# Performance work log

Hardware: AMD Instinct MI355X
Metric: run time of the kernel (lower is better)

The kernel has to match this reference:

```python
import jax, jax.numpy as jnp
import numpy as np

B, S, E = 2, 2048, 4096
H = 16
D = E // H  # 256
MP = 4
ROTARY_DIM = 64
N_POS = 2048


def create_sinusoidal_positions(num_pos, dim):
    inv_freq = 1.0 / (10000.0 ** (jnp.arange(0, dim, 2, dtype=jnp.float32) / dim))
    sinusoid = jnp.einsum('i,j->ij', jnp.arange(num_pos, dtype=jnp.float32), inv_freq)
    return jnp.concatenate([jnp.sin(sinusoid), jnp.cos(sinusoid)], axis=1)  # [num_pos, dim]


def rotate_every_two(x):
    x1 = x[..., ::2]
    x2 = x[..., 1::2]
    return jnp.stack((-x2, x1), axis=-1).reshape(x.shape)


def apply_rotary_pos_emb(t, sin, cos):
    # sin, cos: [B, S, rot/2] -> [B, S, 1, rot] via repeat_interleave(2)
    sin = jnp.repeat(sin[:, :, None, :], 2, axis=-1)
    cos = jnp.repeat(cos[:, :, None, :], 2, axis=-1)
    return t * cos + rotate_every_two(t) * sin


def setup_inputs() -> dict:
    key = jax.random.key(0)
    k1, k2, k3 = jax.random.split(key, 3)
    hidden_states = jax.random.normal(k1, (B, S, E), dtype=jnp.float32) * 0.02
    w_qkv = jax.random.normal(k2, (E, 3 * E), dtype=jnp.float32) * 0.02
    w_out = jax.random.normal(k3, (E, E), dtype=jnp.float32) * 0.02
    position_ids = jnp.tile(jnp.arange(S, dtype=jnp.int32)[None, :], (B, 1))
    return {"hidden_states": hidden_states, "w_qkv": w_qkv, "w_out": w_out,
            "position_ids": position_ids}


def reference(hidden_states, w_qkv, w_out, position_ids):
    qkv = jnp.einsum('bse,ef->bsf', hidden_states, w_qkv)  # [B,S,3E]
    # Moss layout: reshape to mp_num chunks, split order is (query, value, key)
    qkv_split = qkv.reshape(B, S, MP, 3 * E // MP)
    local = D * H // MP
    query = qkv_split[..., :local]
    value = qkv_split[..., local:2 * local]
    key = qkv_split[..., 2 * local:]

    def split_heads(x):  # [B,S,MP,local] -> [B,S,H,D]
        return x.reshape(B, S, MP, H // MP, D).reshape(B, S, H, D)

    query, key, value = split_heads(query), split_heads(key), split_heads(value)

    embed_positions = create_sinusoidal_positions(N_POS, ROTARY_DIM)
    sincos = embed_positions[position_ids]  # [B,S,ROTARY_DIM]
    sin, cos = jnp.split(sincos, 2, axis=-1)

    q_rot = apply_rotary_pos_emb(query[..., :ROTARY_DIM], sin, cos)
    k_rot = apply_rotary_pos_emb(key[..., :ROTARY_DIM], sin, cos)
    query = jnp.concatenate([q_rot, query[..., ROTARY_DIM:]], axis=-1)
    key = jnp.concatenate([k_rot, key[..., ROTARY_DIM:]], axis=-1)

    # fp32 attention with explicit causal mask (faithful to eager source)
    qf = query.astype(jnp.float32)
    kf = key.astype(jnp.float32)
    scale = jnp.sqrt(jnp.float32(D))
    attn_weights = jnp.einsum('bqhd,bkhd->bhqk', qf, kf) / scale  # [B,H,S,S]
    causal = jnp.tril(jnp.ones((S, S), dtype=bool))[None, None]
    mask_value = jnp.finfo(attn_weights.dtype).min
    attn_weights = jnp.where(causal, attn_weights, mask_value)
    attn_weights = jax.nn.softmax(attn_weights, axis=-1).astype(value.dtype)

    attn_output = jnp.einsum('bhqk,bkhd->bqhd', attn_weights, value)  # [B,S,H,D]
    attn_output = attn_output.reshape(B, S, H * D)
    attn_output = jnp.einsum('bse,ef->bsf', attn_output, w_out)
    return attn_output
```

## Files before the change

### kernel.cpp

```cpp
#include <hip/hip_runtime.h>
#include <stdint.h>

typedef unsigned short u16;
typedef __bf16 bf16x8 __attribute__((ext_vector_type(8)));
typedef float f32x4 __attribute__((ext_vector_type(4)));

#define BM 128
#define BN 128
#define BK 32
#define SE 40

__device__ __forceinline__ float bf2f(u16 u) {
    return __uint_as_float(((unsigned int)u) << 16);
}
__device__ __forceinline__ u16 f2bf(float f) {
    unsigned int x = __float_as_uint(f);
    return (u16)((x + 0x7fffu + ((x >> 16) & 1u)) >> 16);
}

__device__ __forceinline__ void ld8(const u16* p, u16* d) {
    *(uint4*)d = *(const uint4*)p;
}
__device__ __forceinline__ void ld8(const float* p, u16* d) {
    float4 a = *(const float4*)p;
    float4 b = *(const float4*)(p + 4);
    d[0] = f2bf(a.x); d[1] = f2bf(a.y); d[2] = f2bf(a.z); d[3] = f2bf(a.w);
    d[4] = f2bf(b.x); d[5] = f2bf(b.y); d[6] = f2bf(b.z); d[7] = f2bf(b.w);
}

__device__ __forceinline__ void stC(u16* p, float v)  { *p = f2bf(v); }
__device__ __forceinline__ void stC(float* p, float v){ *p = v; }

__device__ __forceinline__ void gld_lds16(const u16* g, u16* l) {
    __builtin_amdgcn_global_load_lds(
        (__attribute__((address_space(1))) unsigned int*)(uintptr_t)(const void*)g,
        (__attribute__((address_space(3))) unsigned int*)(uintptr_t)(void*)l,
        16, 0, 0);
}

__device__ __forceinline__ long zoff(int mode, long stride, int hz, int bz) {
    if (mode == 0) return stride * (long)bz;
    if (mode == 1) { int h = hz & 15; return (long)(hz >> 4) * stride + (h >> 2) * 3072 + (h & 3) * 256; }
    if (mode == 3) return stride * (long)hz;
    return (long)(hz >> 4) * stride + (long)(hz & 15) * 256;
}

template <typename TC>
__global__ __launch_bounds__(512, 2) void gemm256(
    const u16* __restrict__ A, long strideAz, int aMode, int lda,
    const u16* __restrict__ B, long strideBz, int bMode, int ldb,
    TC* __restrict__ C, long strideCz, int cMode, int ldc,
    int K, int causal, int zBase)
{
    const int bx = blockIdx.x, by = blockIdx.y, bz = blockIdx.z;
    if (causal == 1 && bx > by) return;
    int kLen = K;
    if (causal == 2) { int kl = (by + 1) * 256; kLen = kl < K ? kl : K; }
    const int NT = kLen >> 6;

    const int hz = bz + zBase;
    const u16* Ab = A + zoff(aMode, strideAz, hz, bz);
    const u16* Bb = B + zoff(bMode, strideBz, hz, bz);
    TC* Cb = C + zoff(cMode, strideCz, hz, bz);

    __shared__ __align__(16) u16 sm[65536];

    const int tid  = threadIdx.x;
    const int lane = tid & 63;
    const int wave = tid >> 6;
    const int quad = lane >> 4;
    const int l16  = lane & 15;
    const int wqm  = wave >> 2;
    const int wqn  = wave & 3;
    const int rowA0 = by * 256;
    const int rowB0 = bx * 256;

    const int sr  = lane >> 3;
    const int sc8 = ((lane & 7) ^ sr) * 8;

    f32x4 acc[2][4][2][2] = {};
    bf16x8 a_r[4][2], b_r[2][2][2];

#define STAGE(G, ld, gr0, kc, smbase) do { \
    _Pragma("unroll") \
    for (int c_ = 0; c_ < 2; ++c_) \
        gld_lds16((G) + (long)((gr0) + c_ * 64 + wave * 8 + sr) * (ld) + ((kc) + sc8), \
                  (smbase) + c_ * 4096 + wave * 512); \
} while (0)

#define ARD(CUR, MH) do { \
    const u16* ab_ = &sm[(CUR) * 16384 + (MH) * 8192]; \
    _Pragma("unroll") for (int i_ = 0; i_ < 4; ++i_) { \
        const int lr_ = wqm * 64 + i_ * 16 + l16; \
        _Pragma("unroll") for (int k_ = 0; k_ < 2; ++k_) \
            a_r[i_][k_] = *(const bf16x8*)(ab_ + lr_ * 64 + (((k_ * 4 + quad) ^ (lr_ & 7)) * 8)); \
    } \
} while (0)

#define BRD(CUR, NH) do { \
    const u16* bb_ = &sm[32768 + (CUR) * 16384 + (NH) * 8192]; \
    _Pragma("unroll") for (int j_ = 0; j_ < 2; ++j_) { \
        const int lr_ = wqn * 32 + j_ * 16 + l16; \
        _Pragma("unroll") for (int k_ = 0; k_ < 2; ++k_) \
            b_r[NH][j_][k_] = *(const bf16x8*)(bb_ + lr_ * 64 + (((k_ * 4 + quad) ^ (lr_ & 7)) * 8)); \
    } \
} while (0)

#define MFMAQ(MH, NH) do { \
    __builtin_amdgcn_s_setprio(1); \
    _Pragma("unroll") for (int i_ = 0; i_ < 4; ++i_) \
    _Pragma("unroll") for (int j_ = 0; j_ < 2; ++j_) \
    _Pragma("unroll") for (int k_ = 0; k_ < 2; ++k_) \
        acc[MH][i_][NH][j_] = __builtin_amdgcn_mfma_f32_16x16x32_bf16( \
            a_r[i_][k_], b_r[NH][j_][k_], acc[MH][i_][NH][j_], 0, 0, 0); \
    __builtin_amdgcn_s_setprio(0); \
} while (0)

#define SB __builtin_amdgcn_sched_barrier(0)
#define BARA do { SB; __builtin_amdgcn_s_barrier(); \
                  asm volatile("s_waitcnt lgkmcnt(0)" ::: "memory"); SB; } while (0)
#define BARB do { SB; __builtin_amdgcn_s_barrier(); SB; } while (0)

    STAGE(Ab, lda, rowA0,       0, &sm[0]);
    STAGE(Bb, ldb, rowB0,       0, &sm[32768]);
    STAGE(Ab, lda, rowA0 + 128, 0, &sm[8192]);
    STAGE(Bb, ldb, rowB0 + 128, 0, &sm[32768 + 8192]);
    STAGE(Ab, lda, rowA0,      64, &sm[16384]);
    STAGE(Bb, ldb, rowB0,      64, &sm[32768 + 16384]);
    asm volatile("s_waitcnt vmcnt(4)" ::: "memory");
    SB; __builtin_amdgcn_s_barrier(); SB;

#define WINDOW(CUR, T) do { \
    ARD(CUR, 0); BRD(CUR, 0); \
    if ((T) + 1 < NT) STAGE(Ab, lda, rowA0 + 128, ((T) + 1) * 64, &sm[(1 - (CUR)) * 16384 + 8192]); \
    BARA; MFMAQ(0, 0); BARB; \
    BRD(CUR, 1); \
    if ((T) + 1 < NT) STAGE(Bb, ldb, rowB0 + 128, ((T) + 1) * 64, &sm[32768 + (1 - (CUR)) * 16384 + 8192]); \
    BARA; MFMAQ(0, 1); BARB; \
    ARD(CUR, 1); \
    if ((T) + 2 < NT) STAGE(Ab, lda, rowA0, ((T) + 2) * 64, &sm[(CUR) * 16384]); \
    BARA; MFMAQ(1, 0); BARB; \
    if ((T) + 2 < NT) { STAGE(Bb, ldb, rowB0, ((T) + 2) * 64, &sm[32768 + (CUR) * 16384]); \
                        asm volatile("s_waitcnt vmcnt(4)" ::: "memory"); } \
    else                asm volatile("s_waitcnt vmcnt(0)" ::: "memory"); \
    BARA; MFMAQ(1, 1); BARB; \
} while (0)

    for (int t = 0; t < NT; t += 2) { WINDOW(0, t); WINDOW(1, t + 1); }

#undef WINDOW
#undef STAGE
#undef ARD
#undef BRD
#undef MFMAQ
#undef SB
#undef BARA
#undef BARB

    #pragma unroll
    for (int mh = 0; mh < 2; ++mh)
    #pragma unroll
    for (int i = 0; i < 4; ++i) {
        const int r0 = rowA0 + mh * 128 + wqm * 64 + i * 16 + quad * 4;
        #pragma unroll
        for (int nh = 0; nh < 2; ++nh)
        #pragma unroll
        for (int j = 0; j < 2; ++j) {
            const int c = rowB0 + nh * 128 + wqn * 32 + j * 16 + l16;
            #pragma unroll
            for (int r = 0; r < 4; ++r)
                stC(&Cb[(long)(r0 + r) * ldc + c], acc[mh][i][nh][j][r]);
        }
    }
}

__global__ __launch_bounds__(256) void cvt_kernel(const float* __restrict__ in,
                                                  u16* __restrict__ out, long n8)
{
    long i = (long)blockIdx.x * 256 + threadIdx.x;
    const long stride = (long)gridDim.x * 256;
    for (; i < n8; i += stride) {
        const float* p = in + i * 8;
        u16 d[8];
        ld8(p, d);
        *(uint4*)(out + i * 8) = *(uint4*)d;
    }
}

__device__ __forceinline__ void ld4(const float* p, u16* d) {
    float4 v = *(const float4*)p;
    d[0] = f2bf(v.x); d[1] = f2bf(v.y); d[2] = f2bf(v.z); d[3] = f2bf(v.w);
}
__device__ __forceinline__ void ld4(const u16* p, u16* d) {
    *(uint2*)d = *(const uint2*)p;
}

template <typename TIn>
__global__ __launch_bounds__(256) void transpose_kernel(
    const TIn* __restrict__ in, int ldin, int inMode, long inZ,
    u16* __restrict__ out, int ldout, long outZ)
{
    __shared__ u16 t[64][68];
    const int bx = blockIdx.x, by = blockIdx.y, bz = blockIdx.z;
    const int h = bz & 15;
    const TIn* inb = in + (inMode == 0 ? inZ * bz
                          : (long)(bz >> 4) * inZ + (long)((h >> 2) * 3072 + 1024 + (h & 3) * 256));
    u16* outb = out + outZ * bz;
    const int tid = threadIdx.x;
    const int r0 = by * 64;
    const int c0 = bx * 64;
    const int lr = tid >> 4;
    const int lc = (tid & 15) * 4;
    #pragma unroll
    for (int i = 0; i < 4; ++i) {
        u16 d[4];
        ld4(inb + (long)(r0 + lr + i * 16) * ldin + (c0 + lc), d);
        *(uint2*)(&t[lr + i * 16][lc]) = *(uint2*)d;
    }
    __syncthreads();
    const int oc  = tid >> 3;
    const int oro = (tid & 7) * 8;
    #pragma unroll
    for (int i = 0; i < 2; ++i) {
        u16 d[8];
        #pragma unroll
        for (int j = 0; j < 8; ++j) d[j] = t[oro + j][oc + i * 32];
        *(uint4*)(outb + (long)(c0 + oc + i * 32) * ldout + (r0 + oro)) = *(uint4*)d;
    }
}

template <bool BT, typename TA, typename TB, typename TC>
__global__ __launch_bounds__(256) void gemm_bf16(
    const TA* __restrict__ A, long strideAz, int aMode, int lda,
    const TB* __restrict__ B, long strideBz, int bMode, int ldb,
    TC* __restrict__ C, long strideCz, int ldc,
    int K, int causal, int zBase)
{
    const int bx = blockIdx.x, by = blockIdx.y, bz = blockIdx.z;
    if (causal == 1 && bx > by) return;
    int kLen = K;
    if (causal == 2) { int kl = (by + 1) * BM; kLen = kl < K ? kl : K; }

    const int hz = bz + zBase;
    const long hoff = (long)((hz >> 2) * 3072 + (hz & 3) * 256);
    const TA* Ab = A + (aMode == 0 ? strideAz * bz : hoff + (long)(aMode - 1) * 1024);
    const TB* Bb = B + (bMode == 0 ? strideBz * bz : hoff + (long)(bMode - 1) * 1024);
    TC* Cb = C + strideCz * bz;

    __shared__ __align__(16) u16 As[BM][SE];
    __shared__ __align__(16) u16 Bs[BN][SE];

    const int tid  = threadIdx.x;
    const int lane = tid & 63;
    const int wave = tid >> 6;
    const int quad = lane >> 4;
    const int l16  = lane & 15;
    const int mBase = (wave >> 1) * 64;
    const int nBase = (wave & 1) * 64;

    const int row0 = by * BM;
    const int col0 = bx * BN;

    const int ar = tid >> 2;
    const int ac = (tid & 3) * 8;
    const int bk = tid & 15;
    const int bg = tid >> 4;

    f32x4 acc[4][4] = {};

    for (int k0 = 0; k0 < kLen; k0 += BK) {
        {
            u16 t0[8], t1[8];
            ld8(Ab + (long)(row0 + ar) * lda + (k0 + ac), t0);
            ld8(Ab + (long)(row0 + ar + 64) * lda + (k0 + ac), t1);
            *(uint4*)(&As[ar][ac])      = *(uint4*)t0;
            *(uint4*)(&As[ar + 64][ac]) = *(uint4*)t1;
        }
        if (BT) {
            u16 t0[8], t1[8];
            ld8(Bb + (long)(col0 + ar) * ldb + (k0 + ac), t0);
            ld8(Bb + (long)(col0 + ar + 64) * ldb + (k0 + ac), t1);
            *(uint4*)(&Bs[ar][ac])      = *(uint4*)t0;
            *(uint4*)(&Bs[ar + 64][ac]) = *(uint4*)t1;
        } else {
            u16 s0[8], s1[8];
            ld8(Bb + (long)(k0 + bk) * ldb + (col0 + bg * 8), s0);
            ld8(Bb + (long)(k0 + bk + 16) * ldb + (col0 + bg * 8), s1);
            #pragma unroll
            for (int j = 0; j < 8; ++j) {
                const int jj = (j + 2 * bg) & 7;
                Bs[bg * 8 + jj][bk]      = s0[jj];
                Bs[bg * 8 + jj][bk + 16] = s1[jj];
            }
        }
        __syncthreads();

        bf16x8 af[4], bfr[4];
        #pragma unroll
        for (int i = 0; i < 4; ++i)
            af[i] = *(const bf16x8*)(&As[mBase + 16 * i + l16][quad * 8]);
        #pragma unroll
        for (int j = 0; j < 4; ++j)
            bfr[j] = *(const bf16x8*)(&Bs[nBase + 16 * j + l16][quad * 8]);
        #pragma unroll
        for (int i = 0; i < 4; ++i)
            #pragma unroll
            for (int j = 0; j < 4; ++j)
                acc[i][j] = __builtin_amdgcn_mfma_f32_16x16x32_bf16(af[i], bfr[j], acc[i][j], 0, 0, 0);
        __syncthreads();
    }

    #pragma unroll
    for (int i = 0; i < 4; ++i) {
        const int r0 = row0 + mBase + 16 * i + quad * 4;
        #pragma unroll
        for (int j = 0; j < 4; ++j) {
            const int c = col0 + nBase + 16 * j + l16;
            #pragma unroll
            for (int r = 0; r < 4; ++r)
                stC(&Cb[(long)(r0 + r) * ldc + c], acc[i][j][r]);
        }
    }
}

__global__ __launch_bounds__(256) void rotary_kernel(u16* __restrict__ qkv,
                                                     const int* __restrict__ pos_ids)
{
    const long bs = blockIdx.x;
    const float pos = (float)pos_ids[bs];
    u16* row = qkv + bs * 12288;
    for (int idx = threadIdx.x; idx < 16 * 224; idx += 256) {
        const int h = idx / 224;
        const int r = idx - h * 224;
        const int base = (h >> 2) * 3072 + (h & 3) * 256;
        if (r < 32) {
            const float invf = powf(10000.0f, (-2.0f * (float)r) * (1.0f / 64.0f));
            float s, c;
            sincosf(pos * invf, &s, &c);
            const int d0 = base + 2 * r;
            const int k0 = d0 + 2048;
            float q0 = bf2f(row[d0]), q1 = bf2f(row[d0 + 1]);
            float ka = bf2f(row[k0]), kb = bf2f(row[k0 + 1]);
            row[d0]     = f2bf((q0 * c - q1 * s) * 0.0625f);
            row[d0 + 1] = f2bf((q1 * c + q0 * s) * 0.0625f);
            row[k0]     = f2bf(ka * c - kb * s);
            row[k0 + 1] = f2bf(kb * c + ka * s);
        } else {
            const int d = base + 64 + (r - 32);
            row[d] = f2bf(bf2f(row[d]) * 0.0625f);
        }
    }
}

__global__ __launch_bounds__(256) void softmax_kernel(u16* __restrict__ scores)
{
    const int qi = blockIdx.x;
    const int h  = blockIdx.y;
    u16* row = scores + ((long)h * 2048 + qi) * 2048;
    const int tid = threadIdx.x;
    const int n = qi + 1;
    const int nc = (qi >> 8) + 1;

    float vals[8];
    float lmax = -3.0e38f;
    #pragma unroll
    for (int i = 0; i < 8; ++i) {
        if (i < nc) {
            const int j = tid + i * 256;
            const float v = (j < n) ? bf2f(row[j]) : -3.0e38f;
            vals[i] = v;
            lmax = fmaxf(lmax, v);
        }
    }
    __shared__ float red[4];
    #pragma unroll
    for (int off = 32; off > 0; off >>= 1) lmax = fmaxf(lmax, __shfl_down(lmax, off));
    if ((tid & 63) == 0) red[tid >> 6] = lmax;
    __syncthreads();
    lmax = fmaxf(fmaxf(red[0], red[1]), fmaxf(red[2], red[3]));

    float lsum = 0.f;
    #pragma unroll
    for (int i = 0; i < 8; ++i) {
        if (i < nc) {
            const int j = tid + i * 256;
            const float e = (j < n) ? expf(vals[i] - lmax) : 0.f;
            vals[i] = e;
            lsum += e;
        }
    }
    #pragma unroll
    for (int off = 32; off > 0; off >>= 1) lsum += __shfl_down(lsum, off);
    __syncthreads();
    if ((tid & 63) == 0) red[tid >> 6] = lsum;
    __syncthreads();
    lsum = red[0] + red[1] + red[2] + red[3];
    const float inv = 1.0f / lsum;
    #pragma unroll
    for (int i = 0; i < 8; ++i)
        if (i < nc) row[tid + i * 256] = f2bf(vals[i] * inv);
}

extern "C" void kernel_launch(void* const* d_in, const int* in_sizes, int n_in,
                              void* d_out, int out_size, void* d_ws, size_t ws_size,
                              hipStream_t stream)
{
    const float* hidden = (const float*)d_in[0];
    const float* w_qkv  = (const float*)d_in[1];
    const float* w_out  = (const float*)d_in[2];
    const int*   pos    = (const int*)d_in[3];
    float* out = (float*)d_out;

    const int Bn = 2, S = 2048, E = 4096, H = 16;
    const int N3 = 3 * E;
    const int Z = Bn * H;
    const size_t per_z = (size_t)S * S * 2;

    dim3 blk(256);
    dim3 blk2(512);

    const size_t fixedA =
        (size_t)N3 * E * 2 +
        (size_t)E * E * 2 +
        (size_t)Bn * S * E * 2 +
        (size_t)Bn * S * N3 * 2 +
        (size_t)Z * 256 * S * 2 +
        (size_t)Bn * S * E * 2;

    if (ws_size >= fixedA + per_z) {
        u16* wqkvT = (u16*)d_ws;
        u16* woutT = wqkvT + (size_t)N3 * E;
        u16* hb    = woutT + (size_t)E * E;
        u16* qkvb  = hb + (size_t)Bn * S * E;
        u16* vT    = qkvb + (size_t)Bn * S * N3;
        u16* attnb = vT + (size_t)Z * 256 * S;
        u16* sc    = attnb + (size_t)Bn * S * E;

        int zc = (int)((ws_size - fixedA) / per_z);
        if (zc > Z) zc = Z;
        while (Z % zc) --zc;

        cvt_kernel<<<dim3(2048), blk, 0, stream>>>(hidden, hb, (long)Bn * S * E / 8);
        transpose_kernel<float><<<dim3(N3 / 64, E / 64, 1), blk, 0, stream>>>(
            w_qkv, N3, 0, 0L, wqkvT, E, 0L);
        transpose_kernel<float><<<dim3(E / 64, E / 64, 1), blk, 0, stream>>>(
            w_out, E, 0, 0L, woutT, E, 0L);

        gemm256<u16><<<dim3(N3 / 256, S / 256, Bn), blk2, 0, stream>>>(
            hb, (long)S * E, 0, E,
            wqkvT, 0L, 0, E,
            qkvb, (long)S * N3, 0, N3, E, 0, 0);

        rotary_kernel<<<dim3(Bn * S), blk, 0, stream>>>(qkvb, pos);

        transpose_kernel<u16><<<dim3(256 / 64, S / 64, Z), blk, 0, stream>>>(
            qkvb, N3, 1, (long)S * N3, vT, S, (long)256 * S);

        for (int z0 = 0; z0 < Z; z0 += zc) {
            gemm256<u16><<<dim3(S / 256, S / 256, zc), blk2, 0, stream>>>(
                qkvb, (long)S * N3, 1, N3,
                qkvb + 2048, (long)S * N3, 1, N3,
                sc, (long)S * S, 0, S,
                256, 1, z0);
            softmax_kernel<<<dim3(S, zc), blk, 0, stream>>>(sc);
            gemm256<u16><<<dim3(1, S / 256, zc), blk2, 0, stream>>>(
                sc, (long)S * S, 0, S,
                vT, (long)256 * S, 3, S,
                attnb, (long)S * E, 4, E,
                S, 2, z0);
        }

        gemm256<float><<<dim3(E / 256, S / 256, Bn), blk2, 0, stream>>>(
            attnb, (long)S * E, 0, E,
            woutT, 0L, 0, E,
            out, (long)S * E, 0, E, E, 0, 0);
        return;
    }

    const size_t fixedB =
        (size_t)N3 * E * 2 +
        (size_t)E * E * 2 +
        (size_t)Bn * S * E * 2 +
        (size_t)S * N3 * 2 +
        (size_t)H * 256 * S * 2 +
        (size_t)S * E * 2;

    if (ws_size >= fixedB + per_z) {
        u16* wqkvT = (u16*)d_ws;
        u16* woutT = wqkvT + (size_t)N3 * E;
        u16* hb    = woutT + (size_t)E * E;
        u16* qkvb  = hb + (size_t)Bn * S * E;
        u16* vT    = qkvb + (size_t)S * N3;
        u16* attnb = vT + (size_t)H * 256 * S;
        u16* sc    = attnb + (size_t)S * E;

        int hc = (int)((ws_size - fixedB) / per_z);
        if (hc > H) hc = H;
        while (H % hc) --hc;

        cvt_kernel<<<dim3(2048), blk, 0, stream>>>(hidden, hb, (long)Bn * S * E / 8);
        transpose_kernel<float><<<dim3(N3 / 64, E / 64, 1), blk, 0, stream>>>(
            w_qkv, N3, 0, 0L, wqkvT, E, 0L);
        transpose_kernel<float><<<dim3(E / 64, E / 64, 1), blk, 0, stream>>>(
            w_out, E, 0, 0L, woutT, E, 0L);

        for (int b = 0; b < Bn; ++b) {
            gemm256<u16><<<dim3(N3 / 256, S / 256, 1), blk2, 0, stream>>>(
                hb + (size_t)b * S * E, 0L, 0, E,
                wqkvT, 0L, 0, E,
                qkvb, 0L, 0, N3, E, 0, 0);

            rotary_kernel<<<dim3(S), blk, 0, stream>>>(qkvb, pos + (size_t)b * S);

            transpose_kernel<u16><<<dim3(256 / 64, S / 64, H), blk, 0, stream>>>(
                qkvb, N3, 1, 0L, vT, S, (long)256 * S);

            for (int h0 = 0; h0 < H; h0 += hc) {
                gemm256<u16><<<dim3(S / 256, S / 256, hc), blk2, 0, stream>>>(
                    qkvb, 0L, 1, N3,
                    qkvb + 2048, 0L, 1, N3,
                    sc, (long)S * S, 0, S,
                    256, 1, h0);
                softmax_kernel<<<dim3(S, hc), blk, 0, stream>>>(sc);
                gemm256<u16><<<dim3(1, S / 256, hc), blk2, 0, stream>>>(
                    sc, (long)S * S, 0, S,
                    vT, (long)256 * S, 3, S,
                    attnb, 0L, 4, E,
                    S, 2, h0);
            }

            gemm256<float><<<dim3(E / 256, S / 256, 1), blk2, 0, stream>>>(
                attnb, 0L, 0, E,
                woutT, 0L, 0, E,
                out + (size_t)b * S * E, 0L, 0, E, E, 0, 0);
        }
        return;
    }

    u16* qkvb  = (u16*)d_ws;
    u16* attnb = qkvb + (size_t)S * N3;
    u16* sc    = attnb + (size_t)S * E;

    const size_t need_base = ((size_t)S * N3 + (size_t)S * E) * 2;
    int hc = 1;
    if (ws_size > need_base) {
        size_t avail = ws_size - need_base;
        hc = (int)(avail / per_z);
        if (hc < 1) hc = 1;
        if (hc > H) hc = H;
        while (H % hc) --hc;
    }

    for (int b = 0; b < Bn; ++b) {
        gemm_bf16<false><<<dim3(N3 / BN, S / BM, 1), blk, 0, stream>>>(
            hidden + (size_t)b * S * E, 0L, 0, E,
            w_qkv, 0L, 0, N3,
            qkvb, 0L, N3, E, 0, 0);

        rotary_kernel<<<dim3(S), blk, 0, stream>>>(qkvb, pos + (size_t)b * S);

        for (int h0 = 0; h0 < H; h0 += hc) {
            gemm_bf16<true><<<dim3(S / BN, S / BM, hc), blk, 0, stream>>>(
                qkvb, 0L, 1, N3,
                qkvb, 0L, 3, N3,
                sc, (long)S * S, S,
                256, 1, h0);
            softmax_kernel<<<dim3(S, hc), blk, 0, stream>>>(sc);
            gemm_bf16<false><<<dim3(2, S / BM, hc), blk, 0, stream>>>(
                sc, (long)S * S, 0, S,
                qkvb, 0L, 2, N3,
                attnb + (size_t)h0 * 256, 256L, E,
                S, 2, h0);
        }

        gemm_bf16<false><<<dim3(E / BN, S / BM, 1), blk, 0, stream>>>(
            attnb, 0L, 0, E,
            w_out, 0L, 0, E,
            out + (size_t)b * S * E, 0L, E, E, 0, 0);
    }
}
```

Before: 1.165 ms.

## Fuse rotary embedding and query scaling into QKV GEMM epilogue, drop trailing barriers

Computes rotary position embedding and the 1/sqrt(D) query scale inside the QKV GEMM store epilogue using sincosf and lane shuffles, removing the separate rotary kernel launch and its extra pass over the QKV buffer. Also removes the second workgroup barrier after each MFMA phase in the main loop to cut synchronisation. Risks: the epilogue adds transcendental math per element, and fewer barriers may allow LDS reuse hazards if the remaining barrier does not fully order reads before overwrites.

```diff
diff --git a/kernel.cpp b/kernel.cpp
--- a/kernel.cpp
+++ b/kernel.cpp
@@ -50,7 +50,7 @@
     const u16* __restrict__ A, long strideAz, int aMode, int lda,
     const u16* __restrict__ B, long strideBz, int bMode, int ldb,
     TC* __restrict__ C, long strideCz, int cMode, int ldc,
-    int K, int causal, int zBase)
+    int K, int causal, int zBase, const int* __restrict__ posids)
 {
     const int bx = blockIdx.x, by = blockIdx.y, bz = blockIdx.z;
     if (causal == 1 && bx > by) return;
@@ -117,9 +117,8 @@
 } while (0)
 
 #define SB __builtin_amdgcn_sched_barrier(0)
-#define BARA do { SB; __builtin_amdgcn_s_barrier(); \
-                  asm volatile("s_waitcnt lgkmcnt(0)" ::: "memory"); SB; } while (0)
-#define BARB do { SB; __builtin_amdgcn_s_barrier(); SB; } while (0)
+#define PHB do { SB; __builtin_amdgcn_s_barrier(); \
+                 asm volatile("s_waitcnt lgkmcnt(0)" ::: "memory"); SB; } while (0)
 
     STAGE(Ab, lda, rowA0,       0, &sm[0]);
     STAGE(Bb, ldb, rowB0,       0, &sm[32768]);
@@ -133,17 +132,17 @@
 #define WINDOW(CUR, T) do { \
     ARD(CUR, 0); BRD(CUR, 0); \
     if ((T) + 1 < NT) STAGE(Ab, lda, rowA0 + 128, ((T) + 1) * 64, &sm[(1 - (CUR)) * 16384 + 8192]); \
-    BARA; MFMAQ(0, 0); BARB; \
+    PHB; MFMAQ(0, 0); \
     BRD(CUR, 1); \
     if ((T) + 1 < NT) STAGE(Bb, ldb, rowB0 + 128, ((T) + 1) * 64, &sm[32768 + (1 - (CUR)) * 16384 + 8192]); \
-    BARA; MFMAQ(0, 1); BARB; \
+    PHB; MFMAQ(0, 1); \
     ARD(CUR, 1); \
     if ((T) + 2 < NT) STAGE(Ab, lda, rowA0, ((T) + 2) * 64, &sm[(CUR) * 16384]); \
-    BARA; MFMAQ(1, 0); BARB; \
+    PHB; MFMAQ(1, 0); \
     if ((T) + 2 < NT) { STAGE(Bb, ldb, rowB0, ((T) + 2) * 64, &sm[32768 + (CUR) * 16384]); \
                         asm volatile("s_waitcnt vmcnt(4)" ::: "memory"); } \
     else                asm volatile("s_waitcnt vmcnt(0)" ::: "memory"); \
-    BARA; MFMAQ(1, 1); BARB; \
+    PHB; MFMAQ(1, 1); \
 } while (0)
 
     for (int t = 0; t < NT; t += 2) { WINDOW(0, t); WINDOW(1, t + 1); }
@@ -154,22 +153,43 @@
 #undef BRD
 #undef MFMAQ
 #undef SB
-#undef BARA
-#undef BARB
+#undef PHB
+
+    const int cm = (bx % 12) >> 2;
+    const bool doRot = (posids != nullptr) && (cm != 1);
+    const float qs = (posids != nullptr && cm == 0) ? 0.0625f : 1.0f;
 
     #pragma unroll
     for (int mh = 0; mh < 2; ++mh)
     #pragma unroll
     for (int i = 0; i < 4; ++i) {
         const int r0 = rowA0 + mh * 128 + wqm * 64 + i * 16 + quad * 4;
-        #pragma unroll
-        for (int nh = 0; nh < 2; ++nh)
-        #pragma unroll
-        for (int j = 0; j < 2; ++j) {
-            const int c = rowB0 + nh * 128 + wqn * 32 + j * 16 + l16;
+        float posv[4];
+        if (doRot) {
             #pragma unroll
             for (int r = 0; r < 4; ++r)
-                stC(&Cb[(long)(r0 + r) * ldc + c], acc[mh][i][nh][j][r]);
+                posv[r] = (float)posids[(long)bz * 2048 + r0 + r];
+        }
+        #pragma unroll
+        for (int nh = 0; nh < 2; ++nh)
+        #pragma unroll
+        for (int j = 0; j < 2; ++j) {
+            const int dcol = nh * 128 + wqn * 32 + j * 16;
+            const int c = rowB0 + dcol + l16;
+            const bool rot = doRot && (dcol < 64);
+            #pragma unroll
+            for (int r = 0; r < 4; ++r) {
+                float v = acc[mh][i][nh][j][r] * qs;
+                if (rot) {
+                    const int d = dcol + l16;
+                    const float invf = powf(10000.0f, (float)(d >> 1) * (-1.0f / 32.0f));
+                    float sn, cs;
+                    sincosf(posv[r] * invf, &sn, &cs);
+                    const float pv = __shfl_xor(v, 1);
+                    v = (d & 1) ? (v * cs + pv * sn) : (v * cs - pv * sn);
+                }
+                stC(&Cb[(long)(r0 + r) * ldc + c], v);
+            }
         }
     }
 }
@@ -449,9 +469,7 @@
         gemm256<u16><<<dim3(N3 / 256, S / 256, Bn), blk2, 0, stream>>>(
             hb, (long)S * E, 0, E,
             wqkvT, 0L, 0, E,
-            qkvb, (long)S * N3, 0, N3, E, 0, 0);
-
-        rotary_kernel<<<dim3(Bn * S), blk, 0, stream>>>(qkvb, pos);
+            qkvb, (long)S * N3, 0, N3, E, 0, 0, pos);
 
         transpose_kernel<u16><<<dim3(256 / 64, S / 64, Z), blk, 0, stream>>>(
             qkvb, N3, 1, (long)S * N3, vT, S, (long)256 * S);
@@ -461,19 +479,19 @@
                 qkvb, (long)S * N3, 1, N3,
                 qkvb + 2048, (long)S * N3, 1, N3,
                 sc, (long)S * S, 0, S,
-                256, 1, z0);
+                256, 1, z0, nullptr);
             softmax_kernel<<<dim3(S, zc), blk, 0, stream>>>(sc);
             gemm256<u16><<<dim3(1, S / 256, zc), blk2, 0, stream>>>(
                 sc, (long)S * S, 0, S,
                 vT, (long)256 * S, 3, S,
                 attnb, (long)S * E, 4, E,
-                S, 2, z0);
+                S, 2, z0, nullptr);
         }
 
         gemm256<float><<<dim3(E / 256, S / 256, Bn), blk2, 0, stream>>>(
             attnb, (long)S * E, 0, E,
             woutT, 0L, 0, E,
-            out, (long)S * E, 0, E, E, 0, 0);
+            out, (long)S * E, 0, E, E, 0, 0, nullptr);
         return;
     }
 
@@ -508,9 +526,7 @@
             gemm256<u16><<<dim3(N3 / 256, S / 256, 1), blk2, 0, stream>>>(
                 hb + (size_t)b * S * E, 0L, 0, E,
                 wqkvT, 0L, 0, E,
-                qkvb, 0L, 0, N3, E, 0, 0);
-
-            rotary_kernel<<<dim3(S), blk, 0, stream>>>(qkvb, pos + (size_t)b * S);
+                qkvb, 0L, 0, N3, E, 0, 0, pos + (size_t)b * S);
 
             transpose_kernel<u16><<<dim3(256 / 64, S / 64, H), blk, 0, stream>>>(
                 qkvb, N3, 1, 0L, vT, S, (long)256 * S);
@@ -520,19 +536,19 @@
                     qkvb, 0L, 1, N3,
                     qkvb + 2048, 0L, 1, N3,
                     sc, (long)S * S, 0, S,
-                    256, 1, h0);
+                    256, 1, h0, nullptr);
                 softmax_kernel<<<dim3(S, hc), blk, 0, stream>>>(sc);
                 gemm256<u16><<<dim3(1, S / 256, hc), blk2, 0, stream>>>(
                     sc, (long)S * S, 0, S,
                     vT, (long)256 * S, 3, S,
                     attnb, 0L, 4, E,
-                    S, 2, h0);
+                    S, 2, h0, nullptr);
             }
 
             gemm256<float><<<dim3(E / 256, S / 256, 1), blk2, 0, stream>>>(
                 attnb, 0L, 0, E,
                 woutT, 0L, 0, E,
-                out + (size_t)b * S * E, 0L, 0, E, E, 0, 0);
+                out + (size_t)b * S * E, 0L, 0, E, E, 0, 0, nullptr);
         }
         return;
     }
```

New measurement: 1.195 ms. 1.03x slower.
